# Kernel tuning notes

Hardware: AMD Instinct MI355X
Metric: run time of the kernel (lower is better)

Reference implementation:

```python
import jax, jax.numpy as jnp
import numpy as np

B, N, C, H = 32, 384, 768, 12
EPS = 1e-6

def setup_inputs() -> dict:
    key = jax.random.key(0)
    k0, k1, k2, k3 = jax.random.split(key, 4)
    x = jax.random.normal(k0, (B, N, C), dtype=jnp.float32)
    # binary keep-mask over key tokens, broadcastable to [B,1,N,N]
    policy = (jax.random.uniform(k1, (B, 1, 1, N)) > 0.5).astype(jnp.float32)
    qkv_w = jax.random.normal(k2, (3 * C, C), dtype=jnp.float32) * 0.02
    qkv_b = jnp.zeros((3 * C,), dtype=jnp.float32)
    proj_w = jax.random.normal(k3, (C, C), dtype=jnp.float32) * 0.02
    proj_b = jnp.zeros((C,), dtype=jnp.float32)
    return {"x": x, "policy": policy, "qkv_w": qkv_w, "qkv_b": qkv_b,
            "proj_w": proj_w, "proj_b": proj_b}

def reference(x, policy, qkv_w, qkv_b, proj_w, proj_b):
    b, n, c = x.shape
    hd = c // H
    scale = hd ** -0.5
    qkv = (x @ qkv_w.T + qkv_b).reshape(b, n, 3, H, hd).transpose(2, 0, 3, 1, 4)
    q, k, v = qkv[0], qkv[1], qkv[2]
    attn = jnp.einsum('bhnd,bhmd->bhnm', q, k) * scale  # [B,H,N,N]
    # softmax_with_policy: eye-blend so every token attends to itself,
    # then eps-regularized masked softmax
    eye = jnp.eye(n, dtype=policy.dtype)[None, None]  # [1,1,N,N]
    attn_policy = policy + (1.0 - policy) * eye       # broadcast -> [B,1,N,N]
    max_att = attn.max(axis=-1, keepdims=True)
    e = jnp.exp(attn - max_att) * attn_policy
    attn = (e + EPS / n) / (e.sum(axis=-1, keepdims=True) + EPS)
    out = jnp.einsum('bhnm,bhmd->bnhd', attn, v).reshape(b, n, c)
    return out @ proj_w.T + proj_b
```

## Files before the change

kernel.cpp:

```cpp
#include <hip/hip_runtime.h>

#define BB 32
#define NN 384
#define CC 768
#define HH 12
#define HD 64

typedef __attribute__((ext_vector_type(4))) float f32x4;
typedef __attribute__((ext_vector_type(8))) __bf16 bf16x8;
typedef __attribute__((ext_vector_type(4))) __bf16 bf16x4;

static __device__ __forceinline__ f32x4 mfma16(bf16x8 a, bf16x8 b, f32x4 c) {
    return __builtin_amdgcn_mfma_f32_16x16x32_bf16(a, b, c, 0, 0, 0);
}

static __device__ __forceinline__ void gload_lds16(const void* g, void* l) {
    __builtin_amdgcn_global_load_lds((const __attribute__((address_space(1))) void*)g,
                                     (__attribute__((address_space(3))) void*)l, 16, 0, 0);
}

#define XU   1179648
#define QU   73728
#define QKVU 221184
#define PU   73728
__global__ void cvt_kernel(const float* __restrict__ x, const float* __restrict__ qkv_w,
                           const float* __restrict__ proj_w, __bf16* __restrict__ dst) {
    const int i = blockIdx.x * blockDim.x + threadIdx.x;
    if (i >= XU + QKVU + PU) return;
    const float* src;
    float sc = 1.f;
    if (i < XU) src = x + (size_t)i * 8;
    else if (i < XU + QKVU) {
        src = qkv_w + (size_t)(i - XU) * 8;
        if (i < XU + QU) sc = 0.125f;
    } else src = proj_w + (size_t)(i - XU - QKVU) * 8;
    f32x4 a = *(const f32x4*)src;
    f32x4 b = *(const f32x4*)(src + 4);
    bf16x8 o;
#pragma unroll
    for (int j = 0; j < 4; ++j) { o[j] = (__bf16)(a[j] * sc); o[j + 4] = (__bf16)(b[j] * sc); }
    *(bf16x8*)(dst + (size_t)i * 8) = o;
}

template <int EPI>
__global__ __launch_bounds__(256, 4) void gemm_kernel(
    const __bf16* __restrict__ A, const __bf16* __restrict__ Bw,
    const float* __restrict__ bias,
    __bf16* __restrict__ qkbuf, __bf16* __restrict__ vtbuf,
    float* __restrict__ fout) {
    __shared__ __bf16 Alds[128 * 64];
    __shared__ __bf16 Blds[128 * 64];

    const int tid = threadIdx.x;
    const int l = tid & 63;
    const int w = tid >> 6;
    const int g = l >> 4, q16 = l & 15;
    const int mb = blockIdx.x * 128;
    const int nb = blockIdx.y * 128;
    const int wrb = (w >> 1) * 64;
    const int wcb = (w & 1) * 64;
    const int srow = w * 8 + (l >> 3);
    const int scol = (l & 7) * 8;

    f32x4 acc[4][4] = {};

    for (int kt = 0; kt < 12; ++kt) {
        const int kof = kt * 64 + scol;
#pragma unroll
        for (int i = 0; i < 4; ++i) {
            gload_lds16(&A[(size_t)(mb + i * 32 + srow) * CC + kof], &Alds[i * 2048 + w * 512]);
            gload_lds16(&Bw[(size_t)(nb + i * 32 + srow) * CC + kof], &Blds[i * 2048 + w * 512]);
        }
        __syncthreads();
#pragma unroll
        for (int c = 0; c < 2; ++c) {
            bf16x8 af[4], bfr[4];
#pragma unroll
            for (int m = 0; m < 4; ++m)
                af[m] = *(const bf16x8*)&Alds[(wrb + m * 16 + q16) * 64 + c * 32 + g * 8];
#pragma unroll
            for (int n = 0; n < 4; ++n)
                bfr[n] = *(const bf16x8*)&Blds[(wcb + n * 16 + q16) * 64 + c * 32 + g * 8];
#pragma unroll
            for (int m = 0; m < 4; ++m)
#pragma unroll
                for (int n = 0; n < 4; ++n)
                    acc[m][n] = mfma16(af[m], bfr[n], acc[m][n]);
        }
        __syncthreads();
    }

    if constexpr (EPI == 0) {
        const int bbatch = mb / NN;
        const int tokb = mb % NN;
#pragma unroll
        for (int n = 0; n < 4; ++n) {
            const int colb = nb + wcb + n * 16;
            const int col = colb + q16;
            float bs = bias[col];
            if (colb < 2 * CC) {
                if (colb < CC) bs *= 0.125f;
#pragma unroll
                for (int m = 0; m < 4; ++m) {
                    const int row = mb + wrb + m * 16 + g * 4;
#pragma unroll
                    for (int r = 0; r < 4; ++r)
                        qkbuf[(size_t)(row + r) * 1536 + col] = (__bf16)(acc[m][n][r] + bs);
                }
            } else {
                const int dd = (col - 2 * CC) & 63;
                const int hh = (colb - 2 * CC) >> 6;
                __bf16* vp = vtbuf + ((size_t)(bbatch * HH + hh) * HD + dd) * NN;
#pragma unroll
                for (int m = 0; m < 4; ++m) {
                    const int tok = tokb + wrb + m * 16 + g * 4;
                    bf16x4 pk;
#pragma unroll
                    for (int r = 0; r < 4; ++r) pk[r] = (__bf16)(acc[m][n][r] + bs);
                    *(bf16x4*)&vp[tok] = pk;
                }
            }
        }
    } else {
#pragma unroll
        for (int n = 0; n < 4; ++n) {
            const int col = nb + wcb + n * 16 + q16;
            const float bs = bias[col];
#pragma unroll
            for (int m = 0; m < 4; ++m)
#pragma unroll
                for (int r = 0; r < 4; ++r)
                    fout[(size_t)(mb + wrb + m * 16 + g * 4 + r) * CC + col] = acc[m][n][r] + bs;
        }
    }
}

__global__ __launch_bounds__(512, 1) void attn_kernel(
    const __bf16* __restrict__ qkbuf, const __bf16* __restrict__ vtbuf,
    const float* __restrict__ policy, __bf16* __restrict__ attb) {
    __shared__ __bf16 Qlds[NN * HD];
    __shared__ __bf16 Klds[NN * HD];
    __shared__ __bf16 Vlds[HD * NN];
    __shared__ float pol[NN];

    const int tid = threadIdx.x;
    const int l = tid & 63;
    const int w = tid >> 6;
    const int g = l >> 4, q16 = l & 15;
    const int bh = blockIdx.x;
    const int b = bh / HH, h = bh % HH;

    const __bf16* qg = qkbuf + (size_t)b * NN * 1536 + h * HD;
    const __bf16* kg = qg + CC;
#pragma unroll
    for (int p = 0; p < 6; ++p) {
        const int cs = p * 512 + w * 64 + l;
        const int row = cs >> 3, cin = cs & 7;
        const size_t go = (size_t)row * 1536 + (size_t)((cin ^ (row & 7)) << 3);
        gload_lds16(&qg[go], &Qlds[(p * 512 + w * 64) * 8]);
        gload_lds16(&kg[go], &Klds[(p * 512 + w * 64) * 8]);
    }
    const __bf16* vg = vtbuf + (size_t)(b * HH + h) * HD * NN;
#pragma unroll
    for (int p = 0; p < 6; ++p) {
        const int cs = p * 512 + w * 64 + l;
        const int row = cs / 48, cin = cs - row * 48;
        gload_lds16(&vg[row * NN + ((cin ^ (row & 7)) << 3)], &Vlds[(p * 512 + w * 64) * 8]);
    }
    for (int i = tid; i < NN; i += 512) pol[i] = policy[b * NN + i];
    __syncthreads();

    const int sw = (q16 & 7) << 4;

    unsigned kw0 = 0, kw1 = 0, kw2 = 0;
#pragma unroll
    for (int kt = 0; kt < 6; ++kt)
#pragma unroll
        for (int t = 0; t < 4; ++t)
#pragma unroll
            for (int r = 0; r < 4; ++r) {
                const int key = kt * 64 + t * 16 + g * 4 + r;
                const unsigned bset = (pol[key] > 0.5f) ? 1u : 0u;
                const int bit = kt * 16 + t * 4 + r;
                if (bit < 32) kw0 |= bset << bit;
                else if (bit < 64) kw1 |= bset << (bit - 32);
                else kw2 |= bset << (bit - 64);
            }

#pragma unroll 1
    for (int ps = 0; ps < 3; ++ps) {
        const int qrow = ps * 128 + w * 16 + q16;
        const int qbyte0 = qrow * 128 + g * 16;
        const bf16x8 qf0 = *(const bf16x8*)((const char*)Qlds + (qbyte0 ^ sw));
        const bf16x8 qf1 = *(const bf16x8*)((const char*)Qlds + ((qbyte0 + 64) ^ sw));

        unsigned pw0 = kw0, pw1 = kw1, pw2 = kw2;
        if (((qrow >> 2) & 3) == g) {
            const int sbit = (qrow >> 6) * 16 + ((qrow >> 4) & 3) * 4 + (qrow & 3);
            if (sbit < 32) pw0 |= 1u << sbit;
            else if (sbit < 64) pw1 |= 1u << (sbit - 32);
            else pw2 |= 1u << (sbit - 64);
        }

        f32x4 oacc[4] = {};
        f32x4 ssum = {0.f, 0.f, 0.f, 0.f};

#pragma unroll 2
        for (int kt = 0; kt < 6; ++kt) {
            f32x4 st[4];
            __builtin_amdgcn_s_setprio(1);
#pragma unroll
            for (int t = 0; t < 4; ++t) {
                const int byte0 = ((kt * 4 + t) * 16 + q16) * 128 + g * 16;
                bf16x8 k0 = *(const bf16x8*)((const char*)Klds + (byte0 ^ sw));
                bf16x8 k1 = *(const bf16x8*)((const char*)Klds + ((byte0 + 64) ^ sw));
                f32x4 z = {0.f, 0.f, 0.f, 0.f};
                st[t] = mfma16(k1, qf1, mfma16(k0, qf0, z));
            }
            __builtin_amdgcn_s_setprio(0);

#pragma unroll
            for (int t = 0; t < 4; ++t) {
#pragma unroll
                for (int r = 0; r < 4; ++r) {
                    const int bit = kt * 16 + t * 4 + r;
                    const unsigned wsel = (bit < 32) ? pw0 : ((bit < 64) ? pw1 : pw2);
                    const bool keep = (wsel >> (bit & 31)) & 1u;
                    st[t][r] = keep ? __expf(st[t][r]) : 0.f;
                }
                ssum += st[t];
            }

            __builtin_amdgcn_s_setprio(1);
#pragma unroll
            for (int c4 = 0; c4 < 2; ++c4) {
                bf16x8 pf;
#pragma unroll
                for (int r = 0; r < 4; ++r) {
                    pf[r] = (__bf16)st[2 * c4][r];
                    pf[r + 4] = (__bf16)st[2 * c4 + 1][r];
                }
                const int c = kt * 2 + c4;
#pragma unroll
                for (int db = 0; db < 4; ++db) {
                    const int byte0 = (db * 16 + q16) * 768 + c * 64 + g * 8;
                    bf16x4 v0 = *(const bf16x4*)((const char*)Vlds + (byte0 ^ sw));
                    bf16x4 v1 = *(const bf16x4*)((const char*)Vlds + ((byte0 + 32) ^ sw));
                    bf16x8 vf;
#pragma unroll
                    for (int r = 0; r < 4; ++r) { vf[r] = v0[r]; vf[r + 4] = v1[r]; }
                    oacc[db] = mfma16(vf, pf, oacc[db]);
                }
            }
            __builtin_amdgcn_s_setprio(0);
        }

        float sum = (ssum[0] + ssum[1]) + (ssum[2] + ssum[3]);
        sum += __shfl_xor(sum, 16);
        sum += __shfl_xor(sum, 32);
        const float dinv = 1.f / (sum + 1e-6f);

        __bf16* op = attb + ((size_t)b * NN + qrow) * CC + h * HD;
#pragma unroll
        for (int db = 0; db < 4; ++db) {
            bf16x4 pk;
#pragma unroll
            for (int r = 0; r < 4; ++r) pk[r] = (__bf16)(oacc[db][r] * dinv);
            *(bf16x4*)&op[db * 16 + g * 4] = pk;
        }
    }
}

extern "C" void kernel_launch(void* const* d_in, const int* in_sizes, int n_in,
                              void* d_out, int out_size, void* d_ws, size_t ws_size,
                              hipStream_t stream) {
    (void)in_sizes; (void)n_in; (void)out_size; (void)ws_size;
    const float* x      = (const float*)d_in[0];
    const float* policy = (const float*)d_in[1];
    const float* qkv_w  = (const float*)d_in[2];
    const float* qkv_b  = (const float*)d_in[3];
    const float* proj_w = (const float*)d_in[4];
    const float* proj_b = (const float*)d_in[5];
    float* out = (float*)d_out;

    __bf16* xb    = (__bf16*)d_ws;
    __bf16* wqkv  = xb + (size_t)12288 * 768;
    __bf16* wproj = wqkv + (size_t)2304 * 768;
    __bf16* qkbuf = wproj + (size_t)768 * 768;
    __bf16* vtbuf = qkbuf + (size_t)12288 * 1536;
    __bf16* attb  = vtbuf + (size_t)BB * HH * HD * NN;

    const int units = XU + QKVU + PU;
    cvt_kernel<<<(units + 255) / 256, 256, 0, stream>>>(x, qkv_w, proj_w, xb);

    gemm_kernel<0><<<dim3(96, 18), 256, 0, stream>>>(xb, wqkv, qkv_b, qkbuf, vtbuf, nullptr);
    attn_kernel<<<384, 512, 0, stream>>>(qkbuf, vtbuf, policy, attb);
    gemm_kernel<1><<<dim3(96, 6), 256, 0, stream>>>(attb, wproj, proj_b, nullptr, nullptr, out);
}
```

Measured before the change: 140.3 us.

## Double-buffer GEMM LDS tiles with XOR swizzle and MFMA priority boost

The QKV/proj GEMM kernel now keeps two LDS buffers per operand and issues the next k-tile's global-to-LDS loads before computing on the current tile, so loads overlap the MFMA work. Global source columns are XOR-swizzled by row so the later fragment reads from LDS avoid bank conflicts. MFMA sections are wrapped in s_setprio. Doubling LDS use lowers the occupancy hint from 4 to 2 blocks per CU, and the loop now relies on one barrier per iteration to keep buffer reuse safe.

```diff
diff --git a/kernel.cpp b/kernel.cpp
--- a/kernel.cpp
+++ b/kernel.cpp
@@ -43,13 +43,13 @@
 }
 
 template <int EPI>
-__global__ __launch_bounds__(256, 4) void gemm_kernel(
+__global__ __launch_bounds__(256, 2) void gemm_kernel(
     const __bf16* __restrict__ A, const __bf16* __restrict__ Bw,
     const float* __restrict__ bias,
     __bf16* __restrict__ qkbuf, __bf16* __restrict__ vtbuf,
     float* __restrict__ fout) {
-    __shared__ __bf16 Alds[128 * 64];
-    __shared__ __bf16 Blds[128 * 64];
+    __shared__ __bf16 SA[2][128 * 64];
+    __shared__ __bf16 SB[2][128 * 64];
 
     const int tid = threadIdx.x;
     const int l = tid & 63;
@@ -59,33 +59,47 @@
     const int nb = blockIdx.y * 128;
     const int wrb = (w >> 1) * 64;
     const int wcb = (w & 1) * 64;
-    const int srow = w * 8 + (l >> 3);
-    const int scol = (l & 7) * 8;
+    const int swz = q16 & 7;
+
+    auto stage = [&](int buf, int kt) {
+#pragma unroll
+        for (int j = 0; j < 4; ++j) {
+            const int ci = j * 256 + w * 64 + l;
+            const int row = ci >> 3, c = ci & 7;
+            const size_t go = (size_t)row * CC + kt * 64 + ((c ^ (row & 7)) << 3);
+            gload_lds16(&A[(size_t)mb * CC + go], &SA[buf][(j * 256 + w * 64) * 8]);
+            gload_lds16(&Bw[(size_t)nb * CC + go], &SB[buf][(j * 256 + w * 64) * 8]);
+        }
+    };
 
     f32x4 acc[4][4] = {};
 
+    stage(0, 0);
+    __syncthreads();
+
     for (int kt = 0; kt < 12; ++kt) {
-        const int kof = kt * 64 + scol;
-#pragma unroll
-        for (int i = 0; i < 4; ++i) {
-            gload_lds16(&A[(size_t)(mb + i * 32 + srow) * CC + kof], &Alds[i * 2048 + w * 512]);
-            gload_lds16(&Bw[(size_t)(nb + i * 32 + srow) * CC + kof], &Blds[i * 2048 + w * 512]);
-        }
-        __syncthreads();
-#pragma unroll
-        for (int c = 0; c < 2; ++c) {
+        const int buf = kt & 1;
+        if (kt < 11) stage(buf ^ 1, kt + 1);
+        const char* pa = (const char*)&SA[buf][0];
+        const char* pb = (const char*)&SB[buf][0];
+#pragma unroll
+        for (int c4 = 0; c4 < 2; ++c4) {
             bf16x8 af[4], bfr[4];
 #pragma unroll
             for (int m = 0; m < 4; ++m)
-                af[m] = *(const bf16x8*)&Alds[(wrb + m * 16 + q16) * 64 + c * 32 + g * 8];
+                af[m] = *(const bf16x8*)(pa + (wrb + m * 16 + q16) * 128 +
+                                         (((c4 * 4 + g) ^ swz) << 4));
 #pragma unroll
             for (int n = 0; n < 4; ++n)
-                bfr[n] = *(const bf16x8*)&Blds[(wcb + n * 16 + q16) * 64 + c * 32 + g * 8];
+                bfr[n] = *(const bf16x8*)(pb + (wcb + n * 16 + q16) * 128 +
+                                          (((c4 * 4 + g) ^ swz) << 4));
+            __builtin_amdgcn_s_setprio(1);
 #pragma unroll
             for (int m = 0; m < 4; ++m)
 #pragma unroll
                 for (int n = 0; n < 4; ++n)
                     acc[m][n] = mfma16(af[m], bfr[n], acc[m][n]);
+            __builtin_amdgcn_s_setprio(0);
         }
         __syncthreads();
     }
```

After: 140.0 us. About the same (-0.2%).
